# Kernel tuning notes

Measured on AMD Instinct MI355X. Metric: run time of the kernel, lower is better.

Reference implementation:

```python
import jax, jax.numpy as jnp
import numpy as np

D_MODEL = 1024
N_HEADS = 16
D_K = D_MODEL // N_HEADS
B, S = 4, 2048


def setup_inputs() -> dict:
    key = jax.random.key(0)
    ks = jax.random.split(key, 9)
    sc = 1.0 / np.sqrt(D_MODEL)
    return {
        "x": jax.random.normal(ks[0], (B, S, D_MODEL), dtype=jnp.float32),
        "Wq": jax.random.normal(ks[1], (D_MODEL, D_MODEL), dtype=jnp.float32) * sc,
        "bq": jax.random.normal(ks[2], (D_MODEL,), dtype=jnp.float32) * 0.02,
        "Wk": jax.random.normal(ks[3], (D_MODEL, D_MODEL), dtype=jnp.float32) * sc,
        "bk": jax.random.normal(ks[4], (D_MODEL,), dtype=jnp.float32) * 0.02,
        "Wv": jax.random.normal(ks[5], (D_MODEL, D_MODEL), dtype=jnp.float32) * sc,
        "bv": jax.random.normal(ks[6], (D_MODEL,), dtype=jnp.float32) * 0.02,
        "Wo": jax.random.normal(ks[7], (D_MODEL, D_MODEL), dtype=jnp.float32) * sc,
        "bo": jax.random.normal(ks[8], (D_MODEL,), dtype=jnp.float32) * 0.02,
    }


def reference(x, Wq, bq, Wk, bk, Wv, bv, Wo, bo):
    b, s, _ = x.shape
    # QKV projections (torch Linear: x @ W.T + b; here weights are stored as [in, out])
    q = (x @ Wq + bq).reshape(b, s, N_HEADS, D_K).transpose(0, 2, 1, 3)  # [b,h,s,dk]
    k = (x @ Wk + bk).reshape(b, s, N_HEADS, D_K).transpose(0, 2, 1, 3)
    v = (x @ Wv + bv).reshape(b, s, N_HEADS, D_K).transpose(0, 2, 1, 3)
    scores = jnp.einsum("bhqd,bhkd->bhqk", q, k) / jnp.sqrt(jnp.float32(D_K))
    attn = jax.nn.softmax(scores, axis=-1)  # dropout=0.0 -> identity
    out = jnp.einsum("bhqk,bhkd->bhqd", attn, v)
    out = out.transpose(0, 2, 1, 3).reshape(b, s, D_MODEL)
    return out @ Wo + bo
```

## Files before the change

kernel.cpp:

```cpp
#include <hip/hip_runtime.h>
#include <hip/hip_bf16.h>

#define DM    1024
#define NH    16
#define DKH   64
#define BB    4
#define SS    2048
#define MROWS (BB*SS)
#define NQK   2048

typedef __attribute__((ext_vector_type(8))) __bf16 bf16x8;
typedef __attribute__((ext_vector_type(4))) float f32x4;
typedef __attribute__((ext_vector_type(16))) float f32x16;
typedef __attribute__((ext_vector_type(4))) unsigned short u16x4;

__device__ __forceinline__ void gload_lds16(const void* g, void* l) {
  __builtin_amdgcn_global_load_lds((const __attribute__((address_space(1))) void*)g,
                                   (__attribute__((address_space(3))) void*)l, 16, 0, 0);
}

__device__ __forceinline__ unsigned short f2bf(float f) {
  __hip_bfloat16 h = __float2bfloat16(f);
  unsigned short u;
  __builtin_memcpy(&u, &h, 2);
  return u;
}

__device__ __forceinline__ unsigned pack2(float a, float b) {
  return (unsigned)f2bf(a) | ((unsigned)f2bf(b) << 16);
}


__global__ __launch_bounds__(256) void cvt_bf16_kernel(const float* __restrict__ in,
                                                       unsigned short* __restrict__ out, int n4) {
  int i = blockIdx.x * 256 + threadIdx.x;
  if (i >= n4) return;
  float4 v = reinterpret_cast<const float4*>(in)[i];
  u16x4 o = { f2bf(v.x), f2bf(v.y), f2bf(v.z), f2bf(v.w) };
  reinterpret_cast<u16x4*>(out)[i] = o;
}

__global__ __launch_bounds__(256) void transpose_cvt4_kernel(
    const float* __restrict__ Wq, const float* __restrict__ Wk,
    const float* __restrict__ Wv, const float* __restrict__ Wo,
    unsigned short* __restrict__ WTqk, unsigned short* __restrict__ WTv,
    unsigned short* __restrict__ WTo) {
  const int z = blockIdx.z;
  const float* W = (z == 0) ? Wq : (z == 1) ? Wk : (z == 2) ? Wv : Wo;
  unsigned short* WT = (z == 0) ? WTqk : (z == 1) ? (WTqk + DM * DM) : (z == 2) ? WTv : WTo;
  __shared__ float t[32][33];
  int tx = threadIdx.x & 31, ty = threadIdx.x >> 5;
  int bx = blockIdx.x * 32, by = blockIdx.y * 32;
#pragma unroll
  for (int i = 0; i < 32; i += 8)
    t[ty + i][tx] = W[(long)(by + ty + i) * DM + bx + tx];
  __syncthreads();
#pragma unroll
  for (int i = 0; i < 32; i += 8)
    WT[(long)(bx + ty + i) * DM + by + tx] = f2bf(t[tx][ty + i]);
}

__global__ void concat2_bias_kernel(const float* __restrict__ a, const float* __restrict__ b,
                                    float* __restrict__ out) {
  int i = blockIdx.x * 256 + threadIdx.x;
  if (i >= NQK) return;
  out[i] = (i < DM) ? a[i] : b[i - DM];
}


template <int MODE>
__global__ __launch_bounds__(256) void gemm_bt_kernel(
    const unsigned short* __restrict__ A,
    const unsigned short* __restrict__ BT,
    const float* __restrict__ bias,
    void* __restrict__ out0, void* __restrict__ out1,
    int M, int N, int K) {
  __shared__ unsigned short As[128 * 32];
  __shared__ unsigned short Bs[128 * 32];
  const int tid = threadIdx.x;
  const int lane = tid & 63;
  const int lr = lane & 15, lg = lane >> 4;
  const int wv = tid >> 6, wm = wv >> 1, wn = wv & 1;
  const long bm = blockIdx.x, bn = blockIdx.y;

  const unsigned short* Ag = A + bm * 128 * K;
  const unsigned short* Bg = BT + bn * 128 * K;

  f32x4 acc[4][4];
#pragma unroll
  for (int i = 0; i < 4; ++i)
#pragma unroll
    for (int j = 0; j < 4; ++j) acc[i][j] = (f32x4){0.f, 0.f, 0.f, 0.f};

  for (int kt = 0; kt < K; kt += 32) {
#pragma unroll
    for (int it = 0; it < 2; ++it) {
      const int e = it * 2048 + tid * 8;
      const int row = e >> 5, col = e & 31;
      gload_lds16(Ag + (long)row * K + kt + col, As + e);
      gload_lds16(Bg + (long)row * K + kt + col, Bs + e);
    }
    __syncthreads();
    bf16x8 af[4], bfr[4];
#pragma unroll
    for (int mi = 0; mi < 4; ++mi)
      af[mi] = *reinterpret_cast<const bf16x8*>(As + (wm * 64 + mi * 16 + lr) * 32 + lg * 8);
#pragma unroll
    for (int ni = 0; ni < 4; ++ni)
      bfr[ni] = *reinterpret_cast<const bf16x8*>(Bs + (wn * 64 + ni * 16 + lr) * 32 + lg * 8);
#pragma unroll
    for (int mi = 0; mi < 4; ++mi)
#pragma unroll
      for (int ni = 0; ni < 4; ++ni)
        acc[mi][ni] = __builtin_amdgcn_mfma_f32_16x16x32_bf16(af[mi], bfr[ni], acc[mi][ni], 0, 0, 0);
    __syncthreads();
  }

  const float QSC = 0.125f * 1.44269504088896340736f;
#pragma unroll
  for (int ni = 0; ni < 4; ++ni) {
    const int col = (int)bn * 128 + wn * 64 + ni * 16 + lr;
    const float bc = (MODE == 1) ? 0.f : bias[col];
#pragma unroll
    for (int mi = 0; mi < 4; ++mi) {
      const int row0 = (int)bm * 128 + wm * 64 + mi * 16 + lg * 4;
#pragma unroll
      for (int r = 0; r < 4; ++r) {
        const int row = row0 + r;
        float v = acc[mi][ni][r] + ((MODE == 1) ? bias[row] : bc);
        if (MODE == 0) {
          if (col < DM) {
            ((unsigned short*)out0)[(long)row * DM + col] = f2bf(v * QSC);
          } else {
            const int c2 = col - DM;
            const int h = c2 >> 6, dh = c2 & 63;
            const int b = row >> 11, s = row & 2047;
            const long idx = ((((long)(b * NH + h) * 32 + (s >> 6)) * 512 +
                               (dh >> 3) * 64 + (s & 63)) << 3) + (dh & 7);
            ((unsigned short*)out1)[idx] = f2bf(v);
          }
        } else if (MODE == 1) {
          const int h = row >> 6, dh = row & 63;
          const int b = col >> 11, s = col & 2047;
          const long idx = ((((long)(b * NH + h) * 32 + (s >> 6)) * 512 +
                             ((s >> 3) & 7) * 64 + dh) << 3) + (s & 7);
          ((unsigned short*)out0)[idx] = f2bf(v);
        } else {
          ((float*)out0)[(long)row * N + col] = v;
        }
      }
    }
  }
}


__global__ __launch_bounds__(256, 3) void attn_kernel(
    const unsigned short* __restrict__ Qb,
    const unsigned short* __restrict__ Kf,
    const unsigned short* __restrict__ Vf,
    unsigned short* __restrict__ AO) {
  __shared__ __align__(16) unsigned short sK[2][4096];
  __shared__ __align__(16) unsigned short sV[2][4096];

  const int tid = threadIdx.x;
  const int lane = tid & 63;
  const int wv = tid >> 6;
  const int q5 = lane & 31;
  const int hi = lane >> 5;

  const int bh = blockIdx.x;
  const int qt = blockIdx.y;
  const int b = bh >> 4, h = bh & 15;

  bf16x8 qf[4];
  {
    const unsigned short* qrow = Qb + (long)(b * SS + qt * 128 + wv * 32 + q5) * DM + h * DKH;
#pragma unroll
    for (int dstep = 0; dstep < 4; ++dstep)
      qf[dstep] = *reinterpret_cast<const bf16x8*>(qrow + dstep * 16 + hi * 8);
  }

  const unsigned short* Kp = Kf + (long)bh * 32 * 4096;
  const unsigned short* Vp = Vf + (long)bh * 32 * 4096;

  f32x16 accv[2];
#pragma unroll
  for (int d = 0; d < 2; ++d)
#pragma unroll
    for (int r = 0; r < 16; ++r) accv[d][r] = 0.f;
  f32x16 lacc;
#pragma unroll
  for (int r = 0; r < 16; ++r) lacc[r] = 0.f;

  f32x16 zc;
#pragma unroll
  for (int r = 0; r < 16; ++r) zc[r] = 0.f;

  auto stage = [&](int buf, int t) {
#pragma unroll
    for (int it = 0; it < 2; ++it) {
      const int u = it * 256 + tid;
      gload_lds16(Kp + (long)t * 4096 + u * 8, &sK[buf][u * 8]);
      gload_lds16(Vp + (long)t * 4096 + u * 8, &sV[buf][u * 8]);
    }
  };

  stage(0, 0);
  __syncthreads();

#pragma unroll 1
  for (int kt = 0; kt < SS / 64; ++kt) {
    const int cur = kt & 1;
    if (kt + 1 < SS / 64) stage(cur ^ 1, kt + 1);
    const unsigned short* K_ = sK[cur];
    const unsigned short* V_ = sV[cur];

    f32x16 s4[2];
    __builtin_amdgcn_s_setprio(1);
#pragma unroll
    for (int kb = 0; kb < 2; ++kb)
#pragma unroll
      for (int dstep = 0; dstep < 4; ++dstep) {
        bf16x8 kf = *reinterpret_cast<const bf16x8*>(
            K_ + ((dstep * 2 + hi) * 64 + kb * 32 + q5) * 8);
        s4[kb] = __builtin_amdgcn_mfma_f32_32x32x16_bf16(kf, qf[dstep],
                                                         dstep ? s4[kb] : zc, 0, 0, 0);
      }
    __builtin_amdgcn_s_setprio(0);

#pragma unroll
    for (int kb = 0; kb < 2; ++kb)
#pragma unroll
      for (int r = 0; r < 16; ++r)
        s4[kb][r] = __builtin_amdgcn_exp2f(s4[kb][r]);
#pragma unroll
    for (int r = 0; r < 16; ++r) lacc[r] += s4[0][r] + s4[1][r];

#pragma unroll
    for (int step = 0; step < 4; ++step) {
      const int kb = step >> 1, rb = (step & 1) * 8;
      const unsigned w0 = pack2(s4[kb][rb + 0], s4[kb][rb + 1]);
      const unsigned w1 = pack2(s4[kb][rb + 2], s4[kb][rb + 3]);
      const unsigned w2 = pack2(s4[kb][rb + 4], s4[kb][rb + 5]);
      const unsigned w3 = pack2(s4[kb][rb + 6], s4[kb][rb + 7]);
      const unsigned c = hi ? w0 : w2;
      const unsigned d = hi ? w1 : w3;
      const unsigned xc = (unsigned)__shfl_xor((int)c, 32);
      const unsigned xd = (unsigned)__shfl_xor((int)d, 32);
      union { unsigned u[4]; bf16x8 v; } pf;
      pf.u[0] = hi ? xc : w0;
      pf.u[1] = hi ? xd : w1;
      pf.u[2] = hi ? w2 : xc;
      pf.u[3] = hi ? w3 : xd;
      __builtin_amdgcn_s_setprio(1);
#pragma unroll
      for (int dblk = 0; dblk < 2; ++dblk) {
        bf16x8 vf = *reinterpret_cast<const bf16x8*>(
            V_ + ((step * 2 + hi) * 64 + dblk * 32 + q5) * 8);
        accv[dblk] = __builtin_amdgcn_mfma_f32_32x32x16_bf16(vf, pf.v, accv[dblk], 0, 0, 0);
      }
      __builtin_amdgcn_s_setprio(0);
    }
    __syncthreads();
  }

  float l01 = (lacc[0] + lacc[1]) + (lacc[2] + lacc[3]);
  float l23 = (lacc[4] + lacc[5]) + (lacc[6] + lacc[7]);
  float l45 = (lacc[8] + lacc[9]) + (lacc[10] + lacc[11]);
  float l67 = (lacc[12] + lacc[13]) + (lacc[14] + lacc[15]);
  float l = (l01 + l23) + (l45 + l67);
  l += __shfl_xor(l, 32);
  const float inv = 1.0f / l;

  const long row = (long)b * SS + qt * 128 + wv * 32 + q5;
  unsigned short* orow = AO + row * DM + h * DKH;
#pragma unroll
  for (int dblk = 0; dblk < 2; ++dblk)
#pragma unroll
    for (int j = 0; j < 8; ++j) {
      const int d0 = dblk * 32 + 8 * (j >> 1) + 4 * hi + 2 * (j & 1);
      const unsigned w = pack2(accv[dblk][2 * j] * inv, accv[dblk][2 * j + 1] * inv);
      *reinterpret_cast<unsigned*>(orow + d0) = w;
    }
}


extern "C" void kernel_launch(void* const* d_in, const int* in_sizes, int n_in,
                              void* d_out, int out_size, void* d_ws, size_t ws_size,
                              hipStream_t stream) {
  const float* x  = (const float*)d_in[0];
  const float* Wq = (const float*)d_in[1];
  const float* bq = (const float*)d_in[2];
  const float* Wk = (const float*)d_in[3];
  const float* bk = (const float*)d_in[4];
  const float* Wv = (const float*)d_in[5];
  const float* bv = (const float*)d_in[6];
  const float* Wo = (const float*)d_in[7];
  const float* bo = (const float*)d_in[8];
  float* out = (float*)d_out;

  char* ws = (char*)d_ws;
  size_t off = 0;
  auto alloc = [&](size_t bytes) {
    void* p = ws + off;
    off += (bytes + 255) & ~(size_t)255;
    return p;
  };
  unsigned short* Xb   = (unsigned short*)alloc((size_t)MROWS * DM * 2);
  unsigned short* WTqk = (unsigned short*)alloc((size_t)2 * DM * DM * 2);
  unsigned short* WTv  = (unsigned short*)alloc((size_t)DM * DM * 2);
  unsigned short* WTo  = (unsigned short*)alloc((size_t)DM * DM * 2);
  float*          bqk  = (float*)alloc((size_t)NQK * 4);
  unsigned short* Qb   = (unsigned short*)alloc((size_t)MROWS * DM * 2);
  unsigned short* Kb2  = (unsigned short*)alloc((size_t)MROWS * DM * 2);
  unsigned short* Vb2  = (unsigned short*)alloc((size_t)MROWS * DM * 2);
  unsigned short* AOb  = (unsigned short*)alloc((size_t)MROWS * DM * 2);

  cvt_bf16_kernel<<<(MROWS * DM / 4 + 255) / 256, 256, 0, stream>>>(x, Xb, MROWS * DM / 4);
  transpose_cvt4_kernel<<<dim3(32, 32, 4), 256, 0, stream>>>(Wq, Wk, Wv, Wo, WTqk, WTv, WTo);
  concat2_bias_kernel<<<(NQK + 255) / 256, 256, 0, stream>>>(bq, bk, bqk);

  gemm_bt_kernel<0><<<dim3(MROWS / 128, NQK / 128), 256, 0, stream>>>(
      Xb, WTqk, bqk, Qb, Kb2, MROWS, NQK, DM);
  gemm_bt_kernel<1><<<dim3(DM / 128, MROWS / 128), 256, 0, stream>>>(
      WTv, Xb, bv, Vb2, nullptr, DM, MROWS, DM);

  attn_kernel<<<dim3(BB * NH, SS / 128), 256, 0, stream>>>(Qb, Kb2, Vb2, AOb);

  gemm_bt_kernel<2><<<dim3(MROWS / 128, DM / 128), 256, 0, stream>>>(
      AOb, WTo, bo, out, nullptr, MROWS, DM, DM);
}
```

Baseline: 241.6 us.

## Process two 32-row query subtiles per wave in attention to reuse K/V fragments

Each wave in the attention kernel now handles 64 query rows (two 32-row subtiles) instead of 32, and each block covers 256 query rows, which halves the grid along the sequence. Every K and V fragment read from LDS feeds two MFMAs instead of one, cutting LDS traffic and global K/V staging per query. The cost is roughly double the accumulator and score registers, so launch bounds drop to 2 blocks per SM. That lowers occupancy and leaves fewer blocks (512) to fill the CUs.

```diff
diff --git a/kernel.cpp b/kernel.cpp
--- a/kernel.cpp
+++ b/kernel.cpp
@@ -11,6 +11,7 @@
 
 typedef __attribute__((ext_vector_type(8))) __bf16 bf16x8;
 typedef __attribute__((ext_vector_type(4))) float f32x4;
+typedef __attribute__((ext_vector_type(8))) float f32x8;
 typedef __attribute__((ext_vector_type(16))) float f32x16;
 typedef __attribute__((ext_vector_type(4))) unsigned short u16x4;
 
@@ -154,7 +155,7 @@
 }
 
 
-__global__ __launch_bounds__(256, 3) void attn_kernel(
+__global__ __launch_bounds__(256, 2) void attn_kernel(
     const unsigned short* __restrict__ Qb,
     const unsigned short* __restrict__ Kf,
     const unsigned short* __restrict__ Vf,
@@ -172,25 +173,31 @@
   const int qt = blockIdx.y;
   const int b = bh >> 4, h = bh & 15;
 
-  bf16x8 qf[4];
-  {
-    const unsigned short* qrow = Qb + (long)(b * SS + qt * 128 + wv * 32 + q5) * DM + h * DKH;
+  bf16x8 qf[2][4];
+#pragma unroll
+  for (int qh = 0; qh < 2; ++qh) {
+    const unsigned short* qrow =
+        Qb + (long)(b * SS + qt * 256 + wv * 64 + qh * 32 + q5) * DM + h * DKH;
 #pragma unroll
     for (int dstep = 0; dstep < 4; ++dstep)
-      qf[dstep] = *reinterpret_cast<const bf16x8*>(qrow + dstep * 16 + hi * 8);
+      qf[qh][dstep] = *reinterpret_cast<const bf16x8*>(qrow + dstep * 16 + hi * 8);
   }
 
   const unsigned short* Kp = Kf + (long)bh * 32 * 4096;
   const unsigned short* Vp = Vf + (long)bh * 32 * 4096;
 
-  f32x16 accv[2];
-#pragma unroll
-  for (int d = 0; d < 2; ++d)
-#pragma unroll
-    for (int r = 0; r < 16; ++r) accv[d][r] = 0.f;
-  f32x16 lacc;
-#pragma unroll
-  for (int r = 0; r < 16; ++r) lacc[r] = 0.f;
+  f32x16 accv[2][2];
+#pragma unroll
+  for (int qh = 0; qh < 2; ++qh)
+#pragma unroll
+    for (int d = 0; d < 2; ++d)
+#pragma unroll
+      for (int r = 0; r < 16; ++r) accv[qh][d][r] = 0.f;
+  f32x8 lacc[2];
+#pragma unroll
+  for (int qh = 0; qh < 2; ++qh)
+#pragma unroll
+    for (int r = 0; r < 8; ++r) lacc[qh][r] = 0.f;
 
   f32x16 zc;
 #pragma unroll
@@ -215,73 +222,90 @@
     const unsigned short* K_ = sK[cur];
     const unsigned short* V_ = sV[cur];
 
-    f32x16 s4[2];
-    __builtin_amdgcn_s_setprio(1);
-#pragma unroll
-    for (int kb = 0; kb < 2; ++kb)
-#pragma unroll
-      for (int dstep = 0; dstep < 4; ++dstep) {
-        bf16x8 kf = *reinterpret_cast<const bf16x8*>(
+    f32x16 s4[2][2];
+#pragma unroll
+    for (int kb = 0; kb < 2; ++kb) {
+      bf16x8 kf[4];
+#pragma unroll
+      for (int dstep = 0; dstep < 4; ++dstep)
+        kf[dstep] = *reinterpret_cast<const bf16x8*>(
             K_ + ((dstep * 2 + hi) * 64 + kb * 32 + q5) * 8);
-        s4[kb] = __builtin_amdgcn_mfma_f32_32x32x16_bf16(kf, qf[dstep],
-                                                         dstep ? s4[kb] : zc, 0, 0, 0);
+      __builtin_amdgcn_s_setprio(1);
+#pragma unroll
+      for (int qh = 0; qh < 2; ++qh)
+#pragma unroll
+        for (int dstep = 0; dstep < 4; ++dstep)
+          s4[qh][kb] = __builtin_amdgcn_mfma_f32_32x32x16_bf16(kf[dstep], qf[qh][dstep],
+                                                               dstep ? s4[qh][kb] : zc, 0, 0, 0);
+      __builtin_amdgcn_s_setprio(0);
+    }
+
+    unsigned pw[2][16];
+#pragma unroll
+    for (int qh = 0; qh < 2; ++qh) {
+#pragma unroll
+      for (int kb = 0; kb < 2; ++kb)
+#pragma unroll
+        for (int r = 0; r < 16; ++r)
+          s4[qh][kb][r] = __builtin_amdgcn_exp2f(s4[qh][kb][r]);
+#pragma unroll
+      for (int j = 0; j < 8; ++j)
+        lacc[qh][j] += (s4[qh][0][j] + s4[qh][0][j + 8]) + (s4[qh][1][j] + s4[qh][1][j + 8]);
+#pragma unroll
+      for (int step = 0; step < 4; ++step) {
+        const int kb = step >> 1, rb = (step & 1) * 8;
+        const unsigned w0 = pack2(s4[qh][kb][rb + 0], s4[qh][kb][rb + 1]);
+        const unsigned w1 = pack2(s4[qh][kb][rb + 2], s4[qh][kb][rb + 3]);
+        const unsigned w2 = pack2(s4[qh][kb][rb + 4], s4[qh][kb][rb + 5]);
+        const unsigned w3 = pack2(s4[qh][kb][rb + 6], s4[qh][kb][rb + 7]);
+        const unsigned c = hi ? w0 : w2;
+        const unsigned d = hi ? w1 : w3;
+        const unsigned xc = (unsigned)__shfl_xor((int)c, 32);
+        const unsigned xd = (unsigned)__shfl_xor((int)d, 32);
+        pw[qh][step * 4 + 0] = hi ? xc : w0;
+        pw[qh][step * 4 + 1] = hi ? xd : w1;
+        pw[qh][step * 4 + 2] = hi ? w2 : xc;
+        pw[qh][step * 4 + 3] = hi ? w3 : xd;
       }
-    __builtin_amdgcn_s_setprio(0);
-
-#pragma unroll
-    for (int kb = 0; kb < 2; ++kb)
-#pragma unroll
-      for (int r = 0; r < 16; ++r)
-        s4[kb][r] = __builtin_amdgcn_exp2f(s4[kb][r]);
-#pragma unroll
-    for (int r = 0; r < 16; ++r) lacc[r] += s4[0][r] + s4[1][r];
+    }
 
 #pragma unroll
     for (int step = 0; step < 4; ++step) {
-      const int kb = step >> 1, rb = (step & 1) * 8;
-      const unsigned w0 = pack2(s4[kb][rb + 0], s4[kb][rb + 1]);
-      const unsigned w1 = pack2(s4[kb][rb + 2], s4[kb][rb + 3]);
-      const unsigned w2 = pack2(s4[kb][rb + 4], s4[kb][rb + 5]);
-      const unsigned w3 = pack2(s4[kb][rb + 6], s4[kb][rb + 7]);
-      const unsigned c = hi ? w0 : w2;
-      const unsigned d = hi ? w1 : w3;
-      const unsigned xc = (unsigned)__shfl_xor((int)c, 32);
-      const unsigned xd = (unsigned)__shfl_xor((int)d, 32);
-      union { unsigned u[4]; bf16x8 v; } pf;
-      pf.u[0] = hi ? xc : w0;
-      pf.u[1] = hi ? xd : w1;
-      pf.u[2] = hi ? w2 : xc;
-      pf.u[3] = hi ? w3 : xd;
+      bf16x8 vf0 = *reinterpret_cast<const bf16x8*>(V_ + ((step * 2 + hi) * 64 + q5) * 8);
+      bf16x8 vf1 = *reinterpret_cast<const bf16x8*>(V_ + ((step * 2 + hi) * 64 + 32 + q5) * 8);
       __builtin_amdgcn_s_setprio(1);
 #pragma unroll
-      for (int dblk = 0; dblk < 2; ++dblk) {
-        bf16x8 vf = *reinterpret_cast<const bf16x8*>(
-            V_ + ((step * 2 + hi) * 64 + dblk * 32 + q5) * 8);
-        accv[dblk] = __builtin_amdgcn_mfma_f32_32x32x16_bf16(vf, pf.v, accv[dblk], 0, 0, 0);
+      for (int qh = 0; qh < 2; ++qh) {
+        union { unsigned u[4]; bf16x8 v; } pf;
+        pf.u[0] = pw[qh][step * 4 + 0];
+        pf.u[1] = pw[qh][step * 4 + 1];
+        pf.u[2] = pw[qh][step * 4 + 2];
+        pf.u[3] = pw[qh][step * 4 + 3];
+        accv[qh][0] = __builtin_amdgcn_mfma_f32_32x32x16_bf16(vf0, pf.v, accv[qh][0], 0, 0, 0);
+        accv[qh][1] = __builtin_amdgcn_mfma_f32_32x32x16_bf16(vf1, pf.v, accv[qh][1], 0, 0, 0);
       }
       __builtin_amdgcn_s_setprio(0);
     }
     __syncthreads();
   }
 
-  float l01 = (lacc[0] + lacc[1]) + (lacc[2] + lacc[3]);
-  float l23 = (lacc[4] + lacc[5]) + (lacc[6] + lacc[7]);
-  float l45 = (lacc[8] + lacc[9]) + (lacc[10] + lacc[11]);
-  float l67 = (lacc[12] + lacc[13]) + (lacc[14] + lacc[15]);
-  float l = (l01 + l23) + (l45 + l67);
-  l += __shfl_xor(l, 32);
-  const float inv = 1.0f / l;
-
-  const long row = (long)b * SS + qt * 128 + wv * 32 + q5;
-  unsigned short* orow = AO + row * DM + h * DKH;
-#pragma unroll
-  for (int dblk = 0; dblk < 2; ++dblk)
-#pragma unroll
-    for (int j = 0; j < 8; ++j) {
-      const int d0 = dblk * 32 + 8 * (j >> 1) + 4 * hi + 2 * (j & 1);
-      const unsigned w = pack2(accv[dblk][2 * j] * inv, accv[dblk][2 * j + 1] * inv);
-      *reinterpret_cast<unsigned*>(orow + d0) = w;
-    }
+#pragma unroll
+  for (int qh = 0; qh < 2; ++qh) {
+    float l = ((lacc[qh][0] + lacc[qh][1]) + (lacc[qh][2] + lacc[qh][3])) +
+              ((lacc[qh][4] + lacc[qh][5]) + (lacc[qh][6] + lacc[qh][7]));
+    l += __shfl_xor(l, 32);
+    const float inv = 1.0f / l;
+    const long row = (long)b * SS + qt * 256 + wv * 64 + qh * 32 + q5;
+    unsigned short* orow = AO + row * DM + h * DKH;
+#pragma unroll
+    for (int dblk = 0; dblk < 2; ++dblk)
+#pragma unroll
+      for (int j = 0; j < 8; ++j) {
+        const int d0 = dblk * 32 + 8 * (j >> 1) + 4 * hi + 2 * (j & 1);
+        const unsigned w = pack2(accv[qh][dblk][2 * j] * inv, accv[qh][dblk][2 * j + 1] * inv);
+        *reinterpret_cast<unsigned*>(orow + d0) = w;
+      }
+  }
 }
 
 
@@ -325,7 +349,7 @@
   gemm_bt_kernel<1><<<dim3(DM / 128, MROWS / 128), 256, 0, stream>>>(
       WTv, Xb, bv, Vb2, nullptr, DM, MROWS, DM);
 
-  attn_kernel<<<dim3(BB * NH, SS / 128), 256, 0, stream>>>(Qb, Kb2, Vb2, AOb);
+  attn_kernel<<<dim3(BB * NH, SS / 256), 256, 0, stream>>>(Qb, Kb2, Vb2, AOb);
 
   gemm_bt_kernel<2><<<dim3(MROWS / 128, DM / 128), 256, 0, stream>>>(
       AOb, WTo, bo, out, nullptr, MROWS, DM, DM);
```

Result: faster. 234.7 us (-2.9%).

## Split attention KV range across two blocks with atomic partial combine

Applied to the files above, without the earlier changes.

Attention blocks now each cover half of the key/value sequence, doubling the grid so the tail wave over the CUs is better balanced. Each block atomically adds its unnormalized fp32 output and row-sum into zeroed workspaces, and a new combine kernel divides by the summed denominator and converts to bf16. This adds two memsets, many scalar fp32 global atomics, and an extra pass over a large fp32 buffer. Merging without a max is safe only because the kernel already skips max subtraction.

```diff
diff --git a/kernel.cpp b/kernel.cpp
--- a/kernel.cpp
+++ b/kernel.cpp
@@ -8,9 +8,11 @@
 #define SS    2048
 #define MROWS (BB*SS)
 #define NQK   2048
+#define NSPLIT 2
 
 typedef __attribute__((ext_vector_type(8))) __bf16 bf16x8;
 typedef __attribute__((ext_vector_type(4))) float f32x4;
+typedef __attribute__((ext_vector_type(8))) float f32x8;
 typedef __attribute__((ext_vector_type(16))) float f32x16;
 typedef __attribute__((ext_vector_type(4))) unsigned short u16x4;
 
@@ -158,7 +160,8 @@
     const unsigned short* __restrict__ Qb,
     const unsigned short* __restrict__ Kf,
     const unsigned short* __restrict__ Vf,
-    unsigned short* __restrict__ AO) {
+    float* __restrict__ Opart,
+    float* __restrict__ lpart) {
   __shared__ __align__(16) unsigned short sK[2][4096];
   __shared__ __align__(16) unsigned short sV[2][4096];
 
@@ -170,6 +173,7 @@
 
   const int bh = blockIdx.x;
   const int qt = blockIdx.y;
+  const int sp = blockIdx.z;
   const int b = bh >> 4, h = bh & 15;
 
   bf16x8 qf[4];
@@ -188,9 +192,9 @@
   for (int d = 0; d < 2; ++d)
 #pragma unroll
     for (int r = 0; r < 16; ++r) accv[d][r] = 0.f;
-  f32x16 lacc;
-#pragma unroll
-  for (int r = 0; r < 16; ++r) lacc[r] = 0.f;
+  f32x8 lacc;
+#pragma unroll
+  for (int r = 0; r < 8; ++r) lacc[r] = 0.f;
 
   f32x16 zc;
 #pragma unroll
@@ -205,13 +209,16 @@
     }
   };
 
-  stage(0, 0);
+  const int NT = SS / 64 / NSPLIT;
+  const int tbase = sp * NT;
+
+  stage(0, tbase);
   __syncthreads();
 
 #pragma unroll 1
-  for (int kt = 0; kt < SS / 64; ++kt) {
+  for (int kt = 0; kt < NT; ++kt) {
     const int cur = kt & 1;
-    if (kt + 1 < SS / 64) stage(cur ^ 1, kt + 1);
+    if (kt + 1 < NT) stage(cur ^ 1, tbase + kt + 1);
     const unsigned short* K_ = sK[cur];
     const unsigned short* V_ = sV[cur];
 
@@ -234,7 +241,8 @@
       for (int r = 0; r < 16; ++r)
         s4[kb][r] = __builtin_amdgcn_exp2f(s4[kb][r]);
 #pragma unroll
-    for (int r = 0; r < 16; ++r) lacc[r] += s4[0][r] + s4[1][r];
+    for (int j = 0; j < 8; ++j)
+      lacc[j] += (s4[0][j] + s4[0][j + 8]) + (s4[1][j] + s4[1][j + 8]);
 
 #pragma unroll
     for (int step = 0; step < 4; ++step) {
@@ -264,24 +272,35 @@
     __syncthreads();
   }
 
-  float l01 = (lacc[0] + lacc[1]) + (lacc[2] + lacc[3]);
-  float l23 = (lacc[4] + lacc[5]) + (lacc[6] + lacc[7]);
-  float l45 = (lacc[8] + lacc[9]) + (lacc[10] + lacc[11]);
-  float l67 = (lacc[12] + lacc[13]) + (lacc[14] + lacc[15]);
-  float l = (l01 + l23) + (l45 + l67);
+  float l = ((lacc[0] + lacc[1]) + (lacc[2] + lacc[3])) +
+            ((lacc[4] + lacc[5]) + (lacc[6] + lacc[7]));
   l += __shfl_xor(l, 32);
-  const float inv = 1.0f / l;
 
   const long row = (long)b * SS + qt * 128 + wv * 32 + q5;
-  unsigned short* orow = AO + row * DM + h * DKH;
+  if (hi == 0) atomicAdd(&lpart[row * NH + h], l);
+  float* orow = Opart + row * DM + h * DKH;
 #pragma unroll
   for (int dblk = 0; dblk < 2; ++dblk)
 #pragma unroll
     for (int j = 0; j < 8; ++j) {
       const int d0 = dblk * 32 + 8 * (j >> 1) + 4 * hi + 2 * (j & 1);
-      const unsigned w = pack2(accv[dblk][2 * j] * inv, accv[dblk][2 * j + 1] * inv);
-      *reinterpret_cast<unsigned*>(orow + d0) = w;
-    }
+      atomicAdd(&orow[d0], accv[dblk][2 * j]);
+      atomicAdd(&orow[d0 + 1], accv[dblk][2 * j + 1]);
+    }
+}
+
+
+__global__ __launch_bounds__(256) void combine_kernel(
+    const float* __restrict__ Opart, const float* __restrict__ lpart,
+    unsigned short* __restrict__ AO) {
+  const long gid = (long)blockIdx.x * 256 + threadIdx.x;
+  const long base = gid * 4;
+  const int row = (int)(base >> 10);
+  const int head = ((int)base & 1023) >> 6;
+  const float4 o = *reinterpret_cast<const float4*>(Opart + base);
+  const float inv = 1.0f / lpart[row * NH + head];
+  u16x4 r = { f2bf(o.x * inv), f2bf(o.y * inv), f2bf(o.z * inv), f2bf(o.w * inv) };
+  *reinterpret_cast<u16x4*>(AO + base) = r;
 }
 
 
@@ -315,6 +334,8 @@
   unsigned short* Kb2  = (unsigned short*)alloc((size_t)MROWS * DM * 2);
   unsigned short* Vb2  = (unsigned short*)alloc((size_t)MROWS * DM * 2);
   unsigned short* AOb  = (unsigned short*)alloc((size_t)MROWS * DM * 2);
+  float*          Opart = (float*)alloc((size_t)MROWS * DM * 4);
+  float*          lpart = (float*)alloc((size_t)MROWS * NH * 4);
 
   cvt_bf16_kernel<<<(MROWS * DM / 4 + 255) / 256, 256, 0, stream>>>(x, Xb, MROWS * DM / 4);
   transpose_cvt4_kernel<<<dim3(32, 32, 4), 256, 0, stream>>>(Wq, Wk, Wv, Wo, WTqk, WTv, WTo);
@@ -325,7 +346,12 @@
   gemm_bt_kernel<1><<<dim3(DM / 128, MROWS / 128), 256, 0, stream>>>(
       WTv, Xb, bv, Vb2, nullptr, DM, MROWS, DM);
 
-  attn_kernel<<<dim3(BB * NH, SS / 128), 256, 0, stream>>>(Qb, Kb2, Vb2, AOb);
+  hipMemsetAsync(Opart, 0, (size_t)MROWS * DM * 4, stream);
+  hipMemsetAsync(lpart, 0, (size_t)MROWS * NH * 4, stream);
+
+  attn_kernel<<<dim3(BB * NH, SS / 128, NSPLIT), 256, 0, stream>>>(Qb, Kb2, Vb2, Opart, lpart);
+
+  combine_kernel<<<MROWS * DM / 4 / 256, 256, 0, stream>>>(Opart, lpart, AOb);
 
   gemm_bt_kernel<2><<<dim3(MROWS / 128, DM / 128), 256, 0, stream>>>(
       AOb, WTo, bo, out, nullptr, MROWS, DM, DM);
```

Result: slower. 629.6 us (+160.6%).
